# Kernel optimization log

Measured on AMD Instinct MI355X. Metric: run time of the kernel, lower is better.

The kernel has to match this reference:

```python
import jax, jax.numpy as jnp
import numpy as np

EPS = 1e-5
HEAD_DIM = 2048 // 32  # embed_dim // num_heads -> scale factor only


def _layernorm(x, w):
    # torch: (x - mean) / sqrt(var_biased + eps) * w  (no bias)
    mean = jnp.mean(x, axis=-1, keepdims=True)
    var = jnp.var(x, axis=-1, keepdims=True)  # unbiased=False
    return w * ((x - mean) / jnp.sqrt(var + EPS))


def setup_inputs() -> dict:
    key = jax.random.key(0)
    ks = jax.random.split(key, 9)
    E, F, B, S = 2048, 8192, 2, 4096
    sE = 1.0 / np.sqrt(E)
    sF = 1.0 / np.sqrt(F)
    return {
        "x": jax.random.normal(ks[0], (B, S, E), jnp.float32),
        "ln_w": jnp.ones((E,), jnp.float32),
        "w_q": jax.random.normal(ks[1], (E, E), jnp.float32) * sE,
        "w_k": jax.random.normal(ks[2], (E, E), jnp.float32) * sE,
        "w_v": jax.random.normal(ks[3], (E, E), jnp.float32) * sE,
        "w_o": jax.random.normal(ks[4], (E, E), jnp.float32) * sE,
        "w_gate": jax.random.normal(ks[5], (E, F), jnp.float32) * sE,
        "w_up": jax.random.normal(ks[6], (E, F), jnp.float32) * sE,
        "w_down": jax.random.normal(ks[7], (F, E), jnp.float32) * sF,
    }


def reference(x, ln_w, w_q, w_k, w_v, w_o, w_gate, w_up, w_down):
    # --- pre-attention LN (uses input_layernorm weight) ---
    residual = x
    h = _layernorm(x, ln_w)  # [b, s, e]

    # --- attention exactly as written: transpose(1,2) WITHOUT head split ---
    q = jnp.einsum("bse,ef->bsf", h, w_q).swapaxes(1, 2)  # [b, e, s]
    k = jnp.einsum("bse,ef->bsf", h, w_k).swapaxes(1, 2)  # [b, e, s]
    v = jnp.einsum("bse,ef->bsf", h, w_v).swapaxes(1, 2)  # [b, e, s]
    # scores over the FEATURE axis: [b, e, e]
    scores = jnp.einsum("bes,bfs->bef", q, k) / np.sqrt(HEAD_DIM)
    weights = jax.nn.softmax(scores, axis=-1)
    attn = jnp.einsum("bef,bfs->bes", weights, v)  # [b, e, s]
    attn = attn.swapaxes(1, 2)  # [b, s, e]
    x = jnp.einsum("bse,ef->bsf", attn, w_o) + residual

    # --- pre-MLP LN: the module reuses input_layernorm here (faithful) ---
    residual = x
    h = _layernorm(x, ln_w)

    # --- GELU-gated FFN (exact erf gelu, torch default) ---
    gate = jax.nn.gelu(jnp.einsum("bse,ef->bsf", h, w_gate), approximate=False)
    up = jnp.einsum("bse,ef->bsf", h, w_up)
    out = jnp.einsum("bsf,fe->bse", gate * up, w_down) + residual
    return out
```

## Files before the change

kernel.cpp:

```cpp
#include <hip/hip_runtime.h>
#include <hip/hip_bf16.h>

typedef __hip_bfloat16 bf16;
typedef __attribute__((ext_vector_type(8))) short bf16x8;
typedef __attribute__((ext_vector_type(4))) float f32x4;

#define EPI_BF16 1
#define EPI_BF16_T 2
#define EPI_F32_RES 3
#define EPI_BF16_GELU 4
#define EPI_BF16_MUL 5
#define EPI_F32_KSPLIT 6

__device__ __forceinline__ void gload_lds16(const bf16* g, char* l) {
  __builtin_amdgcn_global_load_lds(
      (const __attribute__((address_space(1))) unsigned int*)g,
      (__attribute__((address_space(3))) unsigned int*)l, 16, 0, 0);
}

__device__ __forceinline__ unsigned lds_addr(const void* p) {
  return (unsigned)(size_t)(const __attribute__((address_space(3))) char*)p;
}

template<int IMM>
__device__ __forceinline__ bf16x8 dsr(unsigned addr) {
  bf16x8 d;
  asm volatile("ds_read_b128 %0, %1 offset:%c2" : "=v"(d) : "v"(addr), "i"(IMM));
  return d;
}

#define SCHED0() __builtin_amdgcn_sched_barrier(0)
#define VMG(N)                                       \
  do {                                               \
    SCHED0();                                        \
    asm volatile("s_waitcnt vmcnt(" #N ")");         \
    SCHED0();                                        \
  } while (0)
#define BAR_LGKM()                                   \
  do {                                               \
    __builtin_amdgcn_s_barrier();                    \
    SCHED0();                                        \
    asm volatile("s_waitcnt lgkmcnt(0)");            \
    SCHED0();                                        \
  } while (0)

#define RDX(BUF)                                                            \
  do {                                                                      \
    aR[0] = dsr<(BUF) + 0>(aAddr);    aR[1] = dsr<(BUF) + 1024>(aAddr);     \
    aR[2] = dsr<(BUF) + 2048>(aAddr); aR[3] = dsr<(BUF) + 3072>(aAddr);     \
    bR[0] = dsr<(BUF) + 0>(bAddr);    bR[1] = dsr<(BUF) + 1024>(bAddr);     \
    bR[2] = dsr<(BUF) + 2048>(bAddr); bR[3] = dsr<(BUF) + 3072>(bAddr);     \
  } while (0)
#define RDY(BUF)                                                            \
  do {                                                                      \
    aR[0] = dsr<(BUF) + 4096>(aAddr); aR[1] = dsr<(BUF) + 5120>(aAddr);     \
    aR[2] = dsr<(BUF) + 6144>(aAddr); aR[3] = dsr<(BUF) + 7168>(aAddr);     \
  } while (0)

#define MFQH(MB)                                                            \
  do {                                                                      \
    __builtin_amdgcn_s_setprio(1);                                          \
    _Pragma("unroll") for (int mi_ = 0; mi_ < 4; ++mi_)                     \
        _Pragma("unroll") for (int nj_ = 0; nj_ < 4; ++nj_)                 \
            acc[(MB) * 4 + mi_][nj_] =                                      \
                __builtin_amdgcn_mfma_f32_16x16x32_bf16(                    \
                    aR[mi_], bR[nj_], acc[(MB) * 4 + mi_][nj_], 0, 0, 0);   \
    __builtin_amdgcn_s_setprio(0);                                          \
  } while (0)

template<int EPI>
__global__ __launch_bounds__(512, 2) void gemm256_k(
    const bf16* __restrict__ A, const bf16* __restrict__ B,
    void* __restrict__ Cv, const void* __restrict__ auxv,
    int N, int K, int lda, int ldb,
    long sAz, long sBz, long sCz, int batchM)
{
  __shared__ bf16 lds[2 * 4 * 16384 / 2];

  const int gx = gridDim.x, gy = gridDim.y;
  int lid = (blockIdx.z * gy + blockIdx.y) * gx + blockIdx.x;
  const int cpx = (gx * gy * gridDim.z) >> 3;
  lid = (lid & 7) * cpx + (lid >> 3);
  const int bx = lid % gx;
  const int rem = lid / gx;
  const int by = rem % gy;
  const int z = rem / gy;

  int zb = z, part = 0;
  if constexpr (EPI == EPI_F32_KSPLIT) { zb = z & 1; part = z >> 1; }
  A += (size_t)zb * (size_t)sAz + (size_t)part * (size_t)batchM;
  B += (size_t)zb * (size_t)sBz + (size_t)part * (size_t)batchM;

  const int brow = by * 256, bcol = bx * 256;
  const int t = threadIdx.x;
  const int w = t >> 6, lane = t & 63;
  const int wrow = (w >> 2) * 128;
  const int wcol = (w & 3) * 64;
  const int l15 = lane & 15, lg = lane >> 4;

  f32x4 acc[8][4];
#pragma unroll
  for (int i = 0; i < 8; ++i)
#pragma unroll
    for (int j = 0; j < 4; ++j) {
      f32x4 zz = {0.f, 0.f, 0.f, 0.f};
      acc[i][j] = zz;
    }

  auto STAGE1 = [&](int tile, int kh) {
    const int par = tile & 1;
    char* Ad = (char*)lds + (((par << 1) | kh) << 14);
    char* Bd = Ad + 65536;
    const int kk = tile * 64 + kh * 32;
    const int csw = (lane >> 3) & 3;
#pragma unroll
    for (int j = 0; j < 2; ++j) {
      const int bslot = (j * 8 + w) * 64;
      const int slot = bslot + lane;
      const int r = slot >> 2;
      const int cs = (slot & 3) ^ csw;
      gload_lds16(A + (size_t)(brow + r) * lda + kk + cs * 8, Ad + bslot * 16);
      gload_lds16(B + (size_t)(bcol + r) * ldb + kk + cs * 8, Bd + bslot * 16);
    }
  };

  const unsigned chm = (unsigned)((lg ^ ((l15 >> 1) & 3)) * 16);
  const unsigned aAddr = lds_addr(lds) + (unsigned)((wrow + l15) * 64) + chm;
  const unsigned bAddr = lds_addr(lds) + 65536u + (unsigned)((wcol + l15) * 64) + chm;

  STAGE1(0, 0);
  STAGE1(0, 1);
  STAGE1(1, 0);
  VMG(8);
  __builtin_amdgcn_s_barrier();

  const int NT = K >> 6;
  bf16x8 aR[4], bR[4];

  for (int t2 = 0; t2 < NT; t2 += 2) {
    const bool s3 = (t2 + 2) < NT;
    const bool s7 = (t2 + 3) < NT;

    RDX(0);
    STAGE1(t2 + 1, 1);
    BAR_LGKM(); MFQH(0);
    __builtin_amdgcn_s_barrier();
    RDY(0);
    BAR_LGKM(); MFQH(1);
    VMG(8);
    __builtin_amdgcn_s_barrier();
    RDX(16384);
    if (s3) STAGE1(t2 + 2, 0);
    BAR_LGKM(); MFQH(0);
    __builtin_amdgcn_s_barrier();
    RDY(16384);
    BAR_LGKM(); MFQH(1);
    if (s3) VMG(8); else VMG(4);
    __builtin_amdgcn_s_barrier();
    RDX(32768);
    if (s3) STAGE1(t2 + 2, 1);
    BAR_LGKM(); MFQH(0);
    __builtin_amdgcn_s_barrier();
    RDY(32768);
    BAR_LGKM(); MFQH(1);
    if (s3) VMG(8); else VMG(0);
    __builtin_amdgcn_s_barrier();
    RDX(49152);
    if (s7) STAGE1(t2 + 3, 0);
    BAR_LGKM(); MFQH(0);
    __builtin_amdgcn_s_barrier();
    RDY(49152);
    BAR_LGKM(); MFQH(1);
    if (s3) { if (s7) VMG(8); else VMG(4); }
    __builtin_amdgcn_s_barrier();
  }

  if constexpr (EPI == EPI_BF16_T) {
    bf16* C = (bf16*)Cv + (size_t)zb * (size_t)sCz;
#pragma unroll
    for (int mi = 0; mi < 8; ++mi) {
      const int mbase = brow + wrow + mi * 16 + lg * 4;
      const int bi = mbase / batchM;
      const int ms = mbase - bi * batchM;
      const size_t base = (size_t)bi * (size_t)N * (size_t)batchM + (size_t)ms;
#pragma unroll
      for (int ni = 0; ni < 4; ++ni) {
        const int n = bcol + wcol + ni * 16 + l15;
        union { short4 s; short h[4]; } u;
#pragma unroll
        for (int r = 0; r < 4; ++r) {
          bf16 bv = __float2bfloat16(acc[mi][ni][r]);
          u.h[r] = *(short*)&bv;
        }
        *(short4*)(C + base + (size_t)n * (size_t)batchM) = u.s;
      }
    }
  } else {
#pragma unroll
    for (int mi = 0; mi < 8; ++mi) {
#pragma unroll
      for (int r = 0; r < 4; ++r) {
        const int m = brow + wrow + mi * 16 + lg * 4 + r;
#pragma unroll
        for (int ni = 0; ni < 4; ++ni) {
          const int n = bcol + wcol + ni * 16 + l15;
          const size_t idx = (size_t)m * (size_t)N + (size_t)n;
          float v = acc[mi][ni][r];
          if constexpr (EPI == EPI_F32_KSPLIT) {
            float* C = (part ? (float*)auxv : (float*)Cv) + (size_t)zb * (size_t)sCz;
            C[idx] = v;
          } else if constexpr (EPI == EPI_F32_RES) {
            ((float*)Cv)[idx] = v + ((const float*)auxv)[idx];
          } else if constexpr (EPI == EPI_BF16) {
            ((bf16*)Cv)[idx] = __float2bfloat16(v);
          } else if constexpr (EPI == EPI_BF16_GELU) {
            v = 0.5f * v * (1.0f + erff(v * 0.70710678118654752f));
            ((bf16*)Cv)[idx] = __float2bfloat16(v);
          } else if constexpr (EPI == EPI_BF16_MUL) {
            v = v * __bfloat162float(((const bf16*)auxv)[idx]);
            ((bf16*)Cv)[idx] = __float2bfloat16(v);
          }
        }
      }
    }
  }
}

__global__ __launch_bounds__(256) void ln_k(const float* __restrict__ x,
                                            const float* __restrict__ w,
                                            bf16* __restrict__ out) {
  const int row = blockIdx.x;
  const int t = threadIdx.x;
  const float* xr = x + (size_t)row * 2048;
  float4 a = ((const float4*)xr)[2 * t];
  float4 b = ((const float4*)xr)[2 * t + 1];
  float s = a.x + a.y + a.z + a.w + b.x + b.y + b.z + b.w;
  float ss = a.x * a.x + a.y * a.y + a.z * a.z + a.w * a.w +
             b.x * b.x + b.y * b.y + b.z * b.z + b.w * b.w;
#pragma unroll
  for (int o = 1; o < 64; o <<= 1) { s += __shfl_xor(s, o); ss += __shfl_xor(ss, o); }
  __shared__ float ps[4], pss[4];
  if ((t & 63) == 0) { ps[t >> 6] = s; pss[t >> 6] = ss; }
  __syncthreads();
  s = ps[0] + ps[1] + ps[2] + ps[3];
  ss = pss[0] + pss[1] + pss[2] + pss[3];
  const float mean = s * (1.0f / 2048.0f);
  const float var = ss * (1.0f / 2048.0f) - mean * mean;
  const float rstd = rsqrtf(var + 1e-5f);
  float4 wa = ((const float4*)w)[2 * t];
  float4 wb = ((const float4*)w)[2 * t + 1];
  bf16* o8 = out + (size_t)row * 2048 + (size_t)t * 8;
  o8[0] = __float2bfloat16((a.x - mean) * rstd * wa.x);
  o8[1] = __float2bfloat16((a.y - mean) * rstd * wa.y);
  o8[2] = __float2bfloat16((a.z - mean) * rstd * wa.z);
  o8[3] = __float2bfloat16((a.w - mean) * rstd * wa.w);
  o8[4] = __float2bfloat16((b.x - mean) * rstd * wb.x);
  o8[5] = __float2bfloat16((b.y - mean) * rstd * wb.y);
  o8[6] = __float2bfloat16((b.z - mean) * rstd * wb.z);
  o8[7] = __float2bfloat16((b.w - mean) * rstd * wb.w);
}

__global__ __launch_bounds__(256) void softmax2_k(const float* __restrict__ s0,
                                                  const float* __restrict__ s1,
                                                  bf16* __restrict__ o) {
  const int row = blockIdx.x;
  const int t = threadIdx.x;
  const float* r0 = s0 + (size_t)row * 2048;
  const float* r1 = s1 + (size_t)row * 2048;
  float4 a = ((const float4*)r0)[2 * t];
  float4 b = ((const float4*)r0)[2 * t + 1];
  float4 c = ((const float4*)r1)[2 * t];
  float4 d = ((const float4*)r1)[2 * t + 1];
  float v[8] = {a.x + c.x, a.y + c.y, a.z + c.z, a.w + c.w,
                b.x + d.x, b.y + d.y, b.z + d.z, b.w + d.w};
  float m = -1e30f;
#pragma unroll
  for (int i = 0; i < 8; ++i) { v[i] *= 0.125f; m = fmaxf(m, v[i]); }
#pragma unroll
  for (int o2 = 1; o2 < 64; o2 <<= 1) m = fmaxf(m, __shfl_xor(m, o2));
  __shared__ float red[4];
  if ((t & 63) == 0) red[t >> 6] = m;
  __syncthreads();
  m = fmaxf(fmaxf(red[0], red[1]), fmaxf(red[2], red[3]));
  float sum = 0.f;
#pragma unroll
  for (int i = 0; i < 8; ++i) { v[i] = __expf(v[i] - m); sum += v[i]; }
#pragma unroll
  for (int o2 = 1; o2 < 64; o2 <<= 1) sum += __shfl_xor(sum, o2);
  __syncthreads();
  if ((t & 63) == 0) red[t >> 6] = sum;
  __syncthreads();
  sum = red[0] + red[1] + red[2] + red[3];
  const float inv = 1.0f / sum;
  bf16* po = o + (size_t)row * 2048 + (size_t)t * 8;
#pragma unroll
  for (int i = 0; i < 8; ++i) po[i] = __float2bfloat16(v[i] * inv);
}

__global__ __launch_bounds__(256) void transp_k(const float* __restrict__ in,
                                                bf16* __restrict__ out,
                                                int K, int N) {
  __shared__ float tile[32][33];
  const int bn = blockIdx.x * 32;
  const int bk = blockIdx.y * 32;
  const int tx = threadIdx.x;
  const int ty = threadIdx.y;
#pragma unroll
  for (int i = 0; i < 32; i += 8)
    tile[ty + i][tx] = in[(size_t)(bk + ty + i) * N + bn + tx];
  __syncthreads();
#pragma unroll
  for (int i = 0; i < 32; i += 8)
    out[(size_t)(bn + ty + i) * K + bk + tx] = __float2bfloat16(tile[tx][ty + i]);
}

extern "C" void kernel_launch(void* const* d_in, const int* in_sizes, int n_in,
                              void* d_out, int out_size, void* d_ws, size_t ws_size,
                              hipStream_t stream) {
  (void)in_sizes; (void)n_in; (void)out_size; (void)ws_size;
  const float* x   = (const float*)d_in[0];
  const float* lnw = (const float*)d_in[1];
  const float* w_q = (const float*)d_in[2];
  const float* w_k = (const float*)d_in[3];
  const float* w_v = (const float*)d_in[4];
  const float* w_o = (const float*)d_in[5];
  const float* w_g = (const float*)d_in[6];
  const float* w_u = (const float*)d_in[7];
  const float* w_d = (const float*)d_in[8];
  float* out = (float*)d_out;

  const int E = 2048, F = 8192;
  const size_t MB = 1024ull * 1024ull;
  char* ws = (char*)d_ws;

  bf16* wq_t = (bf16*)(ws + 0 * MB);
  bf16* wk_t = (bf16*)(ws + 8 * MB);
  bf16* wv_t = (bf16*)(ws + 16 * MB);
  bf16* wo_t = (bf16*)(ws + 24 * MB);
  bf16* wg_t = (bf16*)(ws + 32 * MB);
  bf16* wu_t = (bf16*)(ws + 64 * MB);
  bf16* wd_t = (bf16*)(ws + 96 * MB);
  bf16*  h   = (bf16*)(ws + 128 * MB);
  float* sp0 = (float*)(ws + 128 * MB);
  bf16*  h2  = (bf16*)(ws + 128 * MB);
  bf16*  qt    = (bf16*)(ws + 160 * MB);
  bf16*  attnT = (bf16*)(ws + 160 * MB);
  bf16*  gc    = (bf16*)(ws + 160 * MB);
  bf16*  kt  = (bf16*)(ws + 192 * MB);
  bf16*  wts = (bf16*)(ws + 192 * MB);
  bf16*  vm  = (bf16*)(ws + 224 * MB);
  float* x2  = (float*)(ws + 224 * MB);
  float* sp1 = (float*)(ws + 256 * MB);

  dim3 blk(256), tb(32, 8), g512(512);

  transp_k<<<dim3(E / 32, E / 32), tb, 0, stream>>>(w_q, wq_t, E, E);
  transp_k<<<dim3(E / 32, E / 32), tb, 0, stream>>>(w_k, wk_t, E, E);
  transp_k<<<dim3(E / 32, E / 32), tb, 0, stream>>>(w_v, wv_t, E, E);
  transp_k<<<dim3(E / 32, E / 32), tb, 0, stream>>>(w_o, wo_t, E, E);
  transp_k<<<dim3(F / 32, E / 32), tb, 0, stream>>>(w_g, wg_t, E, F);
  transp_k<<<dim3(F / 32, E / 32), tb, 0, stream>>>(w_u, wu_t, E, F);
  transp_k<<<dim3(E / 32, F / 32), tb, 0, stream>>>(w_d, wd_t, F, E);

  ln_k<<<8192, blk, 0, stream>>>(x, lnw, h);

  gemm256_k<EPI_BF16_T><<<dim3(8, 32, 1), g512, 0, stream>>>(h, wq_t, qt, nullptr,
      2048, 2048, 2048, 2048, 0, 0, 0, 4096);
  gemm256_k<EPI_BF16_T><<<dim3(8, 32, 1), g512, 0, stream>>>(h, wk_t, kt, nullptr,
      2048, 2048, 2048, 2048, 0, 0, 0, 4096);
  gemm256_k<EPI_BF16><<<dim3(8, 32, 1), g512, 0, stream>>>(h, wv_t, vm, nullptr,
      2048, 2048, 2048, 2048, 0, 0, 0, 1);

  gemm256_k<EPI_F32_KSPLIT><<<dim3(8, 8, 4), g512, 0, stream>>>(qt, kt, sp0, sp1,
      2048, 2048, 4096, 4096, (long)2048 * 4096, (long)2048 * 4096,
      (long)2048 * 2048, 2048);

  softmax2_k<<<4096, blk, 0, stream>>>(sp0, sp1, wts);

  gemm256_k<EPI_BF16_T><<<dim3(16, 8, 2), g512, 0, stream>>>(wts, vm, attnT, nullptr,
      4096, 2048, 2048, 2048, (long)2048 * 2048, (long)4096 * 2048,
      (long)4096 * 2048, 2048);

  gemm256_k<EPI_F32_RES><<<dim3(8, 32, 1), g512, 0, stream>>>(attnT, wo_t, x2, x,
      2048, 2048, 2048, 2048, 0, 0, 0, 1);

  ln_k<<<8192, blk, 0, stream>>>(x2, lnw, h2);

  for (int c = 0; c < 2; ++c) {
    gemm256_k<EPI_BF16_GELU><<<dim3(16, 32, 1), g512, 0, stream>>>(
        h2, wg_t + (size_t)c * 4096 * 2048, gc, nullptr,
        4096, 2048, 2048, 2048, 0, 0, 0, 1);
    gemm256_k<EPI_BF16_MUL><<<dim3(16, 32, 1), g512, 0, stream>>>(
        h2, wu_t + (size_t)c * 4096 * 2048, gc, gc,
        4096, 2048, 2048, 2048, 0, 0, 0, 1);
    gemm256_k<EPI_F32_RES><<<dim3(8, 32, 1), g512, 0, stream>>>(
        gc, wd_t + (size_t)c * 4096, out,
        (c == 0 ? (const void*)x2 : (const void*)out),
        2048, 4096, 4096, 8192, 0, 0, 0, 1);
  }
}
```

Measured before the change: 1.484 ms.

## Switch GEMM inner loop to 32x32x16 MFMA with merged LDS reads per stage

```diff
diff --git a/kernel.cpp b/kernel.cpp
--- a/kernel.cpp
+++ b/kernel.cpp
@@ -3,7 +3,7 @@
 
 typedef __hip_bfloat16 bf16;
 typedef __attribute__((ext_vector_type(8))) short bf16x8;
-typedef __attribute__((ext_vector_type(4))) float f32x4;
+typedef __attribute__((ext_vector_type(16))) float f32x16;
 
 #define EPI_BF16 1
 #define EPI_BF16_T 2
@@ -44,27 +44,29 @@
     SCHED0();                                        \
   } while (0)
 
-#define RDX(BUF)                                                            \
+#define MM(a, b, c) __builtin_amdgcn_mfma_f32_32x32x16_bf16(a, b, c, 0, 0, 0)
+
+#define RD12(SB)                                                            \
   do {                                                                      \
-    aR[0] = dsr<(BUF) + 0>(aAddr);    aR[1] = dsr<(BUF) + 1024>(aAddr);     \
-    aR[2] = dsr<(BUF) + 2048>(aAddr); aR[3] = dsr<(BUF) + 3072>(aAddr);     \
-    bR[0] = dsr<(BUF) + 0>(bAddr);    bR[1] = dsr<(BUF) + 1024>(bAddr);     \
-    bR[2] = dsr<(BUF) + 2048>(bAddr); bR[3] = dsr<(BUF) + 3072>(bAddr);     \
+    aF00 = dsr<(SB) + 0>(aK0);    aF10 = dsr<(SB) + 2048>(aK0);             \
+    aF20 = dsr<(SB) + 4096>(aK0); aF30 = dsr<(SB) + 6144>(aK0);             \
+    bF00 = dsr<(SB) + 0>(bK0);    bF10 = dsr<(SB) + 2048>(bK0);             \
+    aF01 = dsr<(SB) + 0>(aK1);    aF11 = dsr<(SB) + 2048>(aK1);             \
+    aF21 = dsr<(SB) + 4096>(aK1); aF31 = dsr<(SB) + 6144>(aK1);             \
+    bF01 = dsr<(SB) + 0>(bK1);    bF11 = dsr<(SB) + 2048>(bK1);             \
   } while (0)
-#define RDY(BUF)                                                            \
-  do {                                                                      \
-    aR[0] = dsr<(BUF) + 4096>(aAddr); aR[1] = dsr<(BUF) + 5120>(aAddr);     \
-    aR[2] = dsr<(BUF) + 6144>(aAddr); aR[3] = dsr<(BUF) + 7168>(aAddr);     \
-  } while (0)
-
-#define MFQH(MB)                                                            \
+
+#define MF16()                                                              \
   do {                                                                      \
     __builtin_amdgcn_s_setprio(1);                                          \
-    _Pragma("unroll") for (int mi_ = 0; mi_ < 4; ++mi_)                     \
-        _Pragma("unroll") for (int nj_ = 0; nj_ < 4; ++nj_)                 \
-            acc[(MB) * 4 + mi_][nj_] =                                      \
-                __builtin_amdgcn_mfma_f32_16x16x32_bf16(                    \
-                    aR[mi_], bR[nj_], acc[(MB) * 4 + mi_][nj_], 0, 0, 0);   \
+    c00 = MM(aF00, bF00, c00); c01 = MM(aF00, bF10, c01);                   \
+    c10 = MM(aF10, bF00, c10); c11 = MM(aF10, bF10, c11);                   \
+    c20 = MM(aF20, bF00, c20); c21 = MM(aF20, bF10, c21);                   \
+    c30 = MM(aF30, bF00, c30); c31 = MM(aF30, bF10, c31);                   \
+    c00 = MM(aF01, bF01, c00); c01 = MM(aF01, bF11, c01);                   \
+    c10 = MM(aF11, bF01, c10); c11 = MM(aF11, bF11, c11);                   \
+    c20 = MM(aF21, bF01, c20); c21 = MM(aF21, bF11, c21);                   \
+    c30 = MM(aF31, bF01, c30); c31 = MM(aF31, bF11, c31);                   \
     __builtin_amdgcn_s_setprio(0);                                          \
   } while (0)
 
@@ -75,7 +77,7 @@
     int N, int K, int lda, int ldb,
     long sAz, long sBz, long sCz, int batchM)
 {
-  __shared__ bf16 lds[2 * 4 * 16384 / 2];
+  __shared__ bf16 lds[65536];
 
   const int gx = gridDim.x, gy = gridDim.y;
   int lid = (blockIdx.z * gy + blockIdx.y) * gx + blockIdx.x;
@@ -96,37 +98,39 @@
   const int w = t >> 6, lane = t & 63;
   const int wrow = (w >> 2) * 128;
   const int wcol = (w & 3) * 64;
-  const int l15 = lane & 15, lg = lane >> 4;
-
-  f32x4 acc[8][4];
-#pragma unroll
-  for (int i = 0; i < 8; ++i)
-#pragma unroll
-    for (int j = 0; j < 4; ++j) {
-      f32x4 zz = {0.f, 0.f, 0.f, 0.f};
-      acc[i][j] = zz;
-    }
+  const int l31 = lane & 31, lhi = lane >> 5;
+
+  f32x16 z16;
+#pragma unroll
+  for (int i = 0; i < 16; ++i) z16[i] = 0.f;
+  f32x16 c00 = z16, c01 = z16, c10 = z16, c11 = z16,
+         c20 = z16, c21 = z16, c30 = z16, c31 = z16;
+
+  const int csS = (lane & 3) ^ ((lane >> 3) & 3);
+  const int rS0 = w * 16 + (lane >> 2);
+  const int rS1 = (8 + w) * 16 + (lane >> 2);
+  const bf16* pA0 = A + (size_t)(brow + rS0) * lda + csS * 8;
+  const bf16* pA1 = A + (size_t)(brow + rS1) * lda + csS * 8;
+  const bf16* pB0 = B + (size_t)(bcol + rS0) * ldb + csS * 8;
+  const bf16* pB1 = B + (size_t)(bcol + rS1) * ldb + csS * 8;
+  const unsigned ldsOf0 = (unsigned)(w * 64 * 16);
+  const unsigned ldsOf1 = (unsigned)((8 + w) * 64 * 16);
 
   auto STAGE1 = [&](int tile, int kh) {
-    const int par = tile & 1;
-    char* Ad = (char*)lds + (((par << 1) | kh) << 14);
-    char* Bd = Ad + 65536;
+    const int idx = ((tile & 1) << 1) | kh;
+    char* base = (char*)lds + (idx << 14);
     const int kk = tile * 64 + kh * 32;
-    const int csw = (lane >> 3) & 3;
-#pragma unroll
-    for (int j = 0; j < 2; ++j) {
-      const int bslot = (j * 8 + w) * 64;
-      const int slot = bslot + lane;
-      const int r = slot >> 2;
-      const int cs = (slot & 3) ^ csw;
-      gload_lds16(A + (size_t)(brow + r) * lda + kk + cs * 8, Ad + bslot * 16);
-      gload_lds16(B + (size_t)(bcol + r) * ldb + kk + cs * 8, Bd + bslot * 16);
-    }
+    gload_lds16(pA0 + kk, base + ldsOf0);
+    gload_lds16(pB0 + kk, base + 65536 + ldsOf0);
+    gload_lds16(pA1 + kk, base + ldsOf1);
+    gload_lds16(pB1 + kk, base + 65536 + ldsOf1);
   };
 
-  const unsigned chm = (unsigned)((lg ^ ((l15 >> 1) & 3)) * 16);
-  const unsigned aAddr = lds_addr(lds) + (unsigned)((wrow + l15) * 64) + chm;
-  const unsigned bAddr = lds_addr(lds) + 65536u + (unsigned)((wcol + l15) * 64) + chm;
+  const unsigned sw = (unsigned)((lhi ^ ((lane >> 1) & 3)) * 16);
+  const unsigned aK0 = lds_addr(lds) + (unsigned)((wrow + l31) * 64) + sw;
+  const unsigned aK1 = aK0 ^ 32u;
+  const unsigned bK0 = lds_addr(lds) + 65536u + (unsigned)((wcol + l31) * 64) + sw;
+  const unsigned bK1 = bK0 ^ 32u;
 
   STAGE1(0, 0);
   STAGE1(0, 1);
@@ -135,90 +139,93 @@
   __builtin_amdgcn_s_barrier();
 
   const int NT = K >> 6;
-  bf16x8 aR[4], bR[4];
+  bf16x8 aF00, aF10, aF20, aF30, aF01, aF11, aF21, aF31;
+  bf16x8 bF00, bF10, bF01, bF11;
 
   for (int t2 = 0; t2 < NT; t2 += 2) {
     const bool s3 = (t2 + 2) < NT;
     const bool s7 = (t2 + 3) < NT;
 
-    RDX(0);
+    RD12(0);
     STAGE1(t2 + 1, 1);
-    BAR_LGKM(); MFQH(0);
-    __builtin_amdgcn_s_barrier();
-    RDY(0);
-    BAR_LGKM(); MFQH(1);
+    BAR_LGKM();
+    MF16();
     VMG(8);
     __builtin_amdgcn_s_barrier();
-    RDX(16384);
+
+    RD12(16384);
     if (s3) STAGE1(t2 + 2, 0);
-    BAR_LGKM(); MFQH(0);
-    __builtin_amdgcn_s_barrier();
-    RDY(16384);
-    BAR_LGKM(); MFQH(1);
+    BAR_LGKM();
+    MF16();
     if (s3) VMG(8); else VMG(4);
     __builtin_amdgcn_s_barrier();
-    RDX(32768);
+
+    RD12(32768);
     if (s3) STAGE1(t2 + 2, 1);
-    BAR_LGKM(); MFQH(0);
-    __builtin_amdgcn_s_barrier();
-    RDY(32768);
-    BAR_LGKM(); MFQH(1);
+    BAR_LGKM();
+    MF16();
     if (s3) VMG(8); else VMG(0);
     __builtin_amdgcn_s_barrier();
-    RDX(49152);
+
+    RD12(49152);
     if (s7) STAGE1(t2 + 3, 0);
-    BAR_LGKM(); MFQH(0);
-    __builtin_amdgcn_s_barrier();
-    RDY(49152);
-    BAR_LGKM(); MFQH(1);
+    BAR_LGKM();
+    MF16();
     if (s3) { if (s7) VMG(8); else VMG(4); }
     __builtin_amdgcn_s_barrier();
   }
 
+  f32x16 acc[4][2] = {{c00, c01}, {c10, c11}, {c20, c21}, {c30, c31}};
   if constexpr (EPI == EPI_BF16_T) {
     bf16* C = (bf16*)Cv + (size_t)zb * (size_t)sCz;
 #pragma unroll
-    for (int mi = 0; mi < 8; ++mi) {
-      const int mbase = brow + wrow + mi * 16 + lg * 4;
-      const int bi = mbase / batchM;
-      const int ms = mbase - bi * batchM;
-      const size_t base = (size_t)bi * (size_t)N * (size_t)batchM + (size_t)ms;
-#pragma unroll
-      for (int ni = 0; ni < 4; ++ni) {
-        const int n = bcol + wcol + ni * 16 + l15;
-        union { short4 s; short h[4]; } u;
-#pragma unroll
-        for (int r = 0; r < 4; ++r) {
-          bf16 bv = __float2bfloat16(acc[mi][ni][r]);
-          u.h[r] = *(short*)&bv;
+    for (int mi = 0; mi < 4; ++mi) {
+#pragma unroll
+      for (int q = 0; q < 4; ++q) {
+        const int mbase = brow + wrow + mi * 32 + q * 8 + lhi * 4;
+        const int bi = mbase / batchM;
+        const int ms = mbase - bi * batchM;
+        const size_t base = (size_t)bi * (size_t)N * (size_t)batchM + (size_t)ms;
+#pragma unroll
+        for (int ni = 0; ni < 2; ++ni) {
+          const int n = bcol + wcol + ni * 32 + l31;
+          union { short4 s; short h4[4]; } u;
+#pragma unroll
+          for (int r2 = 0; r2 < 4; ++r2) {
+            bf16 bv = __float2bfloat16(acc[mi][ni][q * 4 + r2]);
+            u.h4[r2] = *(short*)&bv;
+          }
+          *(short4*)(C + base + (size_t)n * (size_t)batchM) = u.s;
         }
-        *(short4*)(C + base + (size_t)n * (size_t)batchM) = u.s;
       }
     }
   } else {
 #pragma unroll
-    for (int mi = 0; mi < 8; ++mi) {
-#pragma unroll
-      for (int r = 0; r < 4; ++r) {
-        const int m = brow + wrow + mi * 16 + lg * 4 + r;
-#pragma unroll
-        for (int ni = 0; ni < 4; ++ni) {
-          const int n = bcol + wcol + ni * 16 + l15;
-          const size_t idx = (size_t)m * (size_t)N + (size_t)n;
-          float v = acc[mi][ni][r];
-          if constexpr (EPI == EPI_F32_KSPLIT) {
-            float* C = (part ? (float*)auxv : (float*)Cv) + (size_t)zb * (size_t)sCz;
-            C[idx] = v;
-          } else if constexpr (EPI == EPI_F32_RES) {
-            ((float*)Cv)[idx] = v + ((const float*)auxv)[idx];
-          } else if constexpr (EPI == EPI_BF16) {
-            ((bf16*)Cv)[idx] = __float2bfloat16(v);
-          } else if constexpr (EPI == EPI_BF16_GELU) {
-            v = 0.5f * v * (1.0f + erff(v * 0.70710678118654752f));
-            ((bf16*)Cv)[idx] = __float2bfloat16(v);
-          } else if constexpr (EPI == EPI_BF16_MUL) {
-            v = v * __bfloat162float(((const bf16*)auxv)[idx]);
-            ((bf16*)Cv)[idx] = __float2bfloat16(v);
+    for (int mi = 0; mi < 4; ++mi) {
+#pragma unroll
+      for (int q = 0; q < 4; ++q) {
+#pragma unroll
+        for (int r2 = 0; r2 < 4; ++r2) {
+          const int m = brow + wrow + mi * 32 + q * 8 + lhi * 4 + r2;
+#pragma unroll
+          for (int ni = 0; ni < 2; ++ni) {
+            const int n = bcol + wcol + ni * 32 + l31;
+            const size_t idx = (size_t)m * (size_t)N + (size_t)n;
+            float v = acc[mi][ni][q * 4 + r2];
+            if constexpr (EPI == EPI_F32_KSPLIT) {
+              float* C = (part ? (float*)auxv : (float*)Cv) + (size_t)zb * (size_t)sCz;
+              C[idx] = v;
+            } else if constexpr (EPI == EPI_F32_RES) {
+              ((float*)Cv)[idx] = v + ((const float*)auxv)[idx];
+            } else if constexpr (EPI == EPI_BF16) {
+              ((bf16*)Cv)[idx] = __float2bfloat16(v);
+            } else if constexpr (EPI == EPI_BF16_GELU) {
+              v = 0.5f * v * (1.0f + erff(v * 0.70710678118654752f));
+              ((bf16*)Cv)[idx] = __float2bfloat16(v);
+            } else if constexpr (EPI == EPI_BF16_MUL) {
+              v = v * __bfloat162float(((const bf16*)auxv)[idx]);
+              ((bf16*)Cv)[idx] = __float2bfloat16(v);
+            }
           }
         }
       }
```

New measurement: 1.562 ms. 1.05x slower.

## Reassociate attention via Gram matrix of normalized input and fold W_o into weights

Applied to the files above, without the earlier changes.

```diff
diff --git a/kernel.cpp b/kernel.cpp
--- a/kernel.cpp
+++ b/kernel.cpp
@@ -6,7 +6,6 @@
 typedef __attribute__((ext_vector_type(4))) float f32x4;
 
 #define EPI_BF16 1
-#define EPI_BF16_T 2
 #define EPI_F32_RES 3
 #define EPI_BF16_GELU 4
 #define EPI_BF16_MUL 5
@@ -73,9 +72,9 @@
     const bf16* __restrict__ A, const bf16* __restrict__ B,
     void* __restrict__ Cv, const void* __restrict__ auxv,
     int N, int K, int lda, int ldb,
-    long sAz, long sBz, long sCz, int batchM)
+    long sAz, long sBz, long sCz, int kOff)
 {
-  __shared__ bf16 lds[2 * 4 * 16384 / 2];
+  __shared__ bf16 lds[65536];
 
   const int gx = gridDim.x, gy = gridDim.y;
   int lid = (blockIdx.z * gy + blockIdx.y) * gx + blockIdx.x;
@@ -88,8 +87,8 @@
 
   int zb = z, part = 0;
   if constexpr (EPI == EPI_F32_KSPLIT) { zb = z & 1; part = z >> 1; }
-  A += (size_t)zb * (size_t)sAz + (size_t)part * (size_t)batchM;
-  B += (size_t)zb * (size_t)sBz + (size_t)part * (size_t)batchM;
+  A += (size_t)zb * (size_t)sAz + (size_t)part * (size_t)kOff;
+  B += (size_t)zb * (size_t)sBz + (size_t)part * (size_t)kOff;
 
   const int brow = by * 256, bcol = bx * 256;
   const int t = threadIdx.x;
@@ -175,51 +174,31 @@
     __builtin_amdgcn_s_barrier();
   }
 
-  if constexpr (EPI == EPI_BF16_T) {
-    bf16* C = (bf16*)Cv + (size_t)zb * (size_t)sCz;
-#pragma unroll
-    for (int mi = 0; mi < 8; ++mi) {
-      const int mbase = brow + wrow + mi * 16 + lg * 4;
-      const int bi = mbase / batchM;
-      const int ms = mbase - bi * batchM;
-      const size_t base = (size_t)bi * (size_t)N * (size_t)batchM + (size_t)ms;
+#pragma unroll
+  for (int mi = 0; mi < 8; ++mi) {
+#pragma unroll
+    for (int r = 0; r < 4; ++r) {
+      const int m = brow + wrow + mi * 16 + lg * 4 + r;
 #pragma unroll
       for (int ni = 0; ni < 4; ++ni) {
         const int n = bcol + wcol + ni * 16 + l15;
-        union { short4 s; short h[4]; } u;
-#pragma unroll
-        for (int r = 0; r < 4; ++r) {
-          bf16 bv = __float2bfloat16(acc[mi][ni][r]);
-          u.h[r] = *(short*)&bv;
-        }
-        *(short4*)(C + base + (size_t)n * (size_t)batchM) = u.s;
-      }
-    }
-  } else {
-#pragma unroll
-    for (int mi = 0; mi < 8; ++mi) {
-#pragma unroll
-      for (int r = 0; r < 4; ++r) {
-        const int m = brow + wrow + mi * 16 + lg * 4 + r;
-#pragma unroll
-        for (int ni = 0; ni < 4; ++ni) {
-          const int n = bcol + wcol + ni * 16 + l15;
-          const size_t idx = (size_t)m * (size_t)N + (size_t)n;
-          float v = acc[mi][ni][r];
-          if constexpr (EPI == EPI_F32_KSPLIT) {
-            float* C = (part ? (float*)auxv : (float*)Cv) + (size_t)zb * (size_t)sCz;
-            C[idx] = v;
-          } else if constexpr (EPI == EPI_F32_RES) {
-            ((float*)Cv)[idx] = v + ((const float*)auxv)[idx];
-          } else if constexpr (EPI == EPI_BF16) {
-            ((bf16*)Cv)[idx] = __float2bfloat16(v);
-          } else if constexpr (EPI == EPI_BF16_GELU) {
-            v = 0.5f * v * (1.0f + erff(v * 0.70710678118654752f));
-            ((bf16*)Cv)[idx] = __float2bfloat16(v);
-          } else if constexpr (EPI == EPI_BF16_MUL) {
-            v = v * __bfloat162float(((const bf16*)auxv)[idx]);
-            ((bf16*)Cv)[idx] = __float2bfloat16(v);
-          }
+        const size_t idx = (size_t)m * (size_t)N + (size_t)n;
+        float v = acc[mi][ni][r];
+        if constexpr (EPI == EPI_F32_KSPLIT) {
+          float* C = (part ? (float*)auxv : (float*)Cv) + (size_t)zb * (size_t)sCz;
+          C[idx] = v;
+        } else if constexpr (EPI == EPI_F32_RES) {
+          float* C = (float*)Cv + (size_t)zb * (size_t)sCz;
+          const float* ax = (const float*)auxv + (size_t)zb * (size_t)sCz;
+          C[idx] = v + ax[idx];
+        } else if constexpr (EPI == EPI_BF16) {
+          ((bf16*)Cv)[idx] = __float2bfloat16(v);
+        } else if constexpr (EPI == EPI_BF16_GELU) {
+          v = 0.5f * v * (1.0f + erff(v * 0.70710678118654752f));
+          ((bf16*)Cv)[idx] = __float2bfloat16(v);
+        } else if constexpr (EPI == EPI_BF16_MUL) {
+          v = v * __bfloat162float(((const bf16*)auxv)[idx]);
+          ((bf16*)Cv)[idx] = __float2bfloat16(v);
         }
       }
     }
@@ -314,6 +293,39 @@
     out[(size_t)(bn + ty + i) * K + bk + tx] = __float2bfloat16(tile[tx][ty + i]);
 }
 
+__global__ __launch_bounds__(256) void transb_k(const bf16* __restrict__ in,
+                                                bf16* __restrict__ out,
+                                                int R, int C) {
+  __shared__ bf16 tile[32][34];
+  const size_t zo = (size_t)blockIdx.z * (size_t)R * (size_t)C;
+  in += zo; out += zo;
+  const int bc = blockIdx.x * 32;
+  const int br = blockIdx.y * 32;
+  const int tx = threadIdx.x;
+  const int ty = threadIdx.y;
+#pragma unroll
+  for (int i = 0; i < 32; i += 8)
+    tile[ty + i][tx] = in[(size_t)(br + ty + i) * C + bc + tx];
+  __syncthreads();
+#pragma unroll
+  for (int i = 0; i < 32; i += 8)
+    out[(size_t)(bc + ty + i) * R + br + tx] = tile[tx][ty + i];
+}
+
+__global__ __launch_bounds__(256) void combine_k(const float* __restrict__ a,
+                                                 const float* __restrict__ b,
+                                                 bf16* __restrict__ o, int n4) {
+  int i = blockIdx.x * 256 + threadIdx.x;
+  if (i >= n4) return;
+  float4 x = ((const float4*)a)[i];
+  float4 y = ((const float4*)b)[i];
+  bf16* po = o + (size_t)i * 4;
+  po[0] = __float2bfloat16(x.x + y.x);
+  po[1] = __float2bfloat16(x.y + y.y);
+  po[2] = __float2bfloat16(x.z + y.z);
+  po[3] = __float2bfloat16(x.w + y.w);
+}
+
 extern "C" void kernel_launch(void* const* d_in, const int* in_sizes, int n_in,
                               void* d_out, int out_size, void* d_ws, size_t ws_size,
                               hipStream_t stream) {
@@ -329,7 +341,7 @@
   const float* w_d = (const float*)d_in[8];
   float* out = (float*)d_out;
 
-  const int E = 2048, F = 8192;
+  const int E = 2048, F = 8192, S = 4096;
   const size_t MB = 1024ull * 1024ull;
   char* ws = (char*)d_ws;
 
@@ -340,19 +352,22 @@
   bf16* wg_t = (bf16*)(ws + 32 * MB);
   bf16* wu_t = (bf16*)(ws + 64 * MB);
   bf16* wd_t = (bf16*)(ws + 96 * MB);
-  bf16*  h   = (bf16*)(ws + 128 * MB);
-  float* sp0 = (float*)(ws + 128 * MB);
-  bf16*  h2  = (bf16*)(ws + 128 * MB);
-  bf16*  qt    = (bf16*)(ws + 160 * MB);
-  bf16*  attnT = (bf16*)(ws + 160 * MB);
-  bf16*  gc    = (bf16*)(ws + 160 * MB);
-  bf16*  kt  = (bf16*)(ws + 192 * MB);
-  bf16*  wts = (bf16*)(ws + 192 * MB);
-  bf16*  vm  = (bf16*)(ws + 224 * MB);
-  float* x2  = (float*)(ws + 224 * MB);
-  float* sp1 = (float*)(ws + 256 * MB);
+  bf16*  h    = (bf16*)(ws + 128 * MB);
+  bf16*  h2   = (bf16*)(ws + 128 * MB);
+  bf16*  hT   = (bf16*)(ws + 160 * MB);
+  bf16*  Gb   = (bf16*)(ws + 160 * MB);
+  bf16*  wts  = (bf16*)(ws + 160 * MB);
+  bf16*  T1b  = (bf16*)(ws + 176 * MB);
+  bf16*  wtsT = (bf16*)(ws + 176 * MB);
+  bf16*  UT   = (bf16*)(ws + 176 * MB);
+  bf16*  gc   = (bf16*)(ws + 160 * MB);
+  bf16*  vm   = (bf16*)(ws + 192 * MB);
+  float* p0   = (float*)(ws + 224 * MB);
+  float* p1   = (float*)(ws + 256 * MB);
+  float* x2   = (float*)(ws + 224 * MB);
 
   dim3 blk(256), tb(32, 8), g512(512);
+  const long EE = (long)E * E;
 
   transp_k<<<dim3(E / 32, E / 32), tb, 0, stream>>>(w_q, wq_t, E, E);
   transp_k<<<dim3(E / 32, E / 32), tb, 0, stream>>>(w_k, wk_t, E, E);
@@ -364,38 +379,44 @@
 
   ln_k<<<8192, blk, 0, stream>>>(x, lnw, h);
 
-  gemm256_k<EPI_BF16_T><<<dim3(8, 32, 1), g512, 0, stream>>>(h, wq_t, qt, nullptr,
-      2048, 2048, 2048, 2048, 0, 0, 0, 4096);
-  gemm256_k<EPI_BF16_T><<<dim3(8, 32, 1), g512, 0, stream>>>(h, wk_t, kt, nullptr,
-      2048, 2048, 2048, 2048, 0, 0, 0, 4096);
+  transb_k<<<dim3(E / 32, S / 32, 2), tb, 0, stream>>>(h, hT, S, E);
+
   gemm256_k<EPI_BF16><<<dim3(8, 32, 1), g512, 0, stream>>>(h, wv_t, vm, nullptr,
-      2048, 2048, 2048, 2048, 0, 0, 0, 1);
-
-  gemm256_k<EPI_F32_KSPLIT><<<dim3(8, 8, 4), g512, 0, stream>>>(qt, kt, sp0, sp1,
-      2048, 2048, 4096, 4096, (long)2048 * 4096, (long)2048 * 4096,
-      (long)2048 * 2048, 2048);
-
-  softmax2_k<<<4096, blk, 0, stream>>>(sp0, sp1, wts);
-
-  gemm256_k<EPI_BF16_T><<<dim3(16, 8, 2), g512, 0, stream>>>(wts, vm, attnT, nullptr,
-      4096, 2048, 2048, 2048, (long)2048 * 2048, (long)4096 * 2048,
-      (long)4096 * 2048, 2048);
-
-  gemm256_k<EPI_F32_RES><<<dim3(8, 32, 1), g512, 0, stream>>>(attnT, wo_t, x2, x,
-      2048, 2048, 2048, 2048, 0, 0, 0, 1);
+      E, E, E, E, 0, 0, 0, 0);
+
+  gemm256_k<EPI_F32_KSPLIT><<<dim3(8, 8, 4), g512, 0, stream>>>(hT, hT, p0, p1,
+      E, 2048, S, S, (long)E * S, (long)E * S, EE, 2048);
+  combine_k<<<dim3(2 * E * E / 1024), blk, 0, stream>>>(p0, p1, Gb, 2 * E * E / 4);
+
+  gemm256_k<EPI_F32_KSPLIT><<<dim3(8, 8, 4), g512, 0, stream>>>(wq_t, Gb, p0, p1,
+      E, 1024, E, E, 0, EE, EE, 1024);
+  combine_k<<<dim3(2 * E * E / 1024), blk, 0, stream>>>(p0, p1, T1b, 2 * E * E / 4);
+
+  gemm256_k<EPI_F32_KSPLIT><<<dim3(8, 8, 4), g512, 0, stream>>>(T1b, wk_t, p0, p1,
+      E, 1024, E, E, EE, 0, EE, 1024);
+  softmax2_k<<<4096, blk, 0, stream>>>(p0, p1, wts);
+
+  transb_k<<<dim3(E / 32, E / 32, 2), tb, 0, stream>>>(wts, wtsT, E, E);
+
+  gemm256_k<EPI_F32_KSPLIT><<<dim3(8, 8, 4), g512, 0, stream>>>(wo_t, wtsT, p0, p1,
+      E, 1024, E, E, 0, EE, EE, 1024);
+  combine_k<<<dim3(2 * E * E / 1024), blk, 0, stream>>>(p0, p1, UT, 2 * E * E / 4);
+
+  gemm256_k<EPI_F32_RES><<<dim3(8, 16, 2), g512, 0, stream>>>(vm, UT, x2, x,
+      E, E, E, E, (long)S * E, EE, (long)S * E, 0);
 
   ln_k<<<8192, blk, 0, stream>>>(x2, lnw, h2);
 
   for (int c = 0; c < 2; ++c) {
     gemm256_k<EPI_BF16_GELU><<<dim3(16, 32, 1), g512, 0, stream>>>(
         h2, wg_t + (size_t)c * 4096 * 2048, gc, nullptr,
-        4096, 2048, 2048, 2048, 0, 0, 0, 1);
+        4096, E, E, E, 0, 0, 0, 0);
     gemm256_k<EPI_BF16_MUL><<<dim3(16, 32, 1), g512, 0, stream>>>(
         h2, wu_t + (size_t)c * 4096 * 2048, gc, gc,
-        4096, 2048, 2048, 2048, 0, 0, 0, 1);
+        4096, E, E, E, 0, 0, 0, 0);
     gemm256_k<EPI_F32_RES><<<dim3(8, 32, 1), g512, 0, stream>>>(
         gc, wd_t + (size_t)c * 4096, out,
         (c == 0 ? (const void*)x2 : (const void*)out),
-        2048, 4096, 4096, 8192, 0, 0, 0, 1);
+        E, 4096, 4096, F, 0, 0, 0, 0);
   }
 }
```

Result: faster. 1.450 ms (-2.3%).
